# Kernel optimization log

Hardware: AMD Instinct MI355X
Metric: run time of the kernel (lower is better)

## Reference

```python
import jax, jax.numpy as jnp
import numpy as np

HEADS = 4
DIM_HEAD = 32
GROUPS = 32  # min(256//4, 32)
EPS = 1e-5


def setup_inputs() -> dict:
    key = jax.random.key(0)
    ks = jax.random.split(key, 6)
    B, C, H, W = 16, 256, 64, 64
    hidden = HEADS * DIM_HEAD  # 128
    return {
        "x": jax.random.normal(ks[0], (B, C, H, W), dtype=jnp.float32),
        "gn_w": jax.random.uniform(ks[1], (C,), dtype=jnp.float32),
        "gn_b": jax.random.normal(ks[2], (C,), dtype=jnp.float32) * 0.05,
        "qkv_w": jax.random.normal(ks[3], (3 * hidden, C), dtype=jnp.float32) * 0.05,
        "qkv_b": jax.random.normal(ks[4], (3 * hidden,), dtype=jnp.float32) * 0.05,
        "out_w": jax.random.normal(ks[5], (C, hidden), dtype=jnp.float32) * 0.05,
        "out_b": jnp.zeros((C,), dtype=jnp.float32),
    }


def _forward_single(x, gn_w, gn_b, qkv_w, qkv_b, out_w, out_b):
    # x: (c, h, w)
    c, h, w = x.shape
    # GroupNorm over (channels-in-group, h, w)
    xg = x.reshape(GROUPS, c // GROUPS, h, w)
    mean = xg.mean(axis=(1, 2, 3), keepdims=True)
    var = xg.var(axis=(1, 2, 3), keepdims=True)
    xn = ((xg - mean) * jax.lax.rsqrt(var + EPS)).reshape(c, h, w)
    xn = xn * gn_w[:, None, None] + gn_b[:, None, None]
    # 1x1 conv QKV projection
    qkv = jnp.einsum('oc,chw->ohw', qkv_w, xn) + qkv_b[:, None, None]
    qkv = qkv.reshape(3, HEADS, DIM_HEAD, h * w)
    q, k, v = qkv[0], qkv[1], qkv[2]
    k = jax.nn.softmax(k, axis=-1)  # softmax over spatial
    context = jnp.einsum('hdn,hen->hde', k, v)   # (heads, d, d)
    out = jnp.einsum('hde,hdn->hen', context, q)  # (heads, d, n)
    out = out.reshape(HEADS * DIM_HEAD, h, w)
    # 1x1 conv output projection
    return jnp.einsum('oc,chw->ohw', out_w, out) + out_b[:, None, None]


def reference(x, gn_w, gn_b, qkv_w, qkv_b, out_w, out_b):
    f = lambda xi: _forward_single(xi, gn_w, gn_b, qkv_w, qkv_b, out_w, out_b)
    return jax.vmap(f)(x)
```

## Files before the change

kernel.cpp:

```cpp
#include <hip/hip_runtime.h>
#include <stdint.h>

typedef unsigned short u16;
typedef __attribute__((ext_vector_type(8))) short bf16x8;
typedef __attribute__((ext_vector_type(4))) float f32x4;

#define B_   16
#define C_   256
#define HW_  4096
#define QR_  384
#define HID_ 128

__device__ __forceinline__ float b2f(u16 u) {
  union { uint32_t i; float f; } v; v.i = ((uint32_t)u) << 16; return v.f;
}
__device__ __forceinline__ u16 f2b(float f) {
  union { float f; uint32_t i; } v; v.f = f;
  uint32_t r = (v.i + 0x7FFFu + ((v.i >> 16) & 1u)) >> 16;
  return (u16)r;
}

__global__ __launch_bounds__(256) void gn_stats_conv_kernel(
    const float* __restrict__ x, const float* __restrict__ gnw,
    const float* __restrict__ gnb, float* __restrict__ scale,
    float* __restrict__ shiftv,
    const float* __restrict__ qkvw, u16* __restrict__ cqkvw)
{
  if (blockIdx.x >= 512) {
    int i = (blockIdx.x - 512) * 256 + threadIdx.x;
    float4 f = ((const float4*)qkvw)[i];
    ushort4 o;
    o.x = f2b(f.x); o.y = f2b(f.y); o.z = f2b(f.z); o.w = f2b(f.w);
    ((ushort4*)cqkvw)[i] = o;
    return;
  }
  int b = blockIdx.x >> 5, g = blockIdx.x & 31;
  const float* p = x + ((size_t)b * C_ + g * 8) * HW_;
  int t = threadIdx.x;
  float s = 0.f, sq = 0.f;
#pragma unroll
  for (int i = 0; i < 16; ++i) {
    float4 u0 = *(const float4*)(p + t * 8 + i * 2048);
    float4 u1 = *(const float4*)(p + t * 8 + i * 2048 + 4);
    s  += u0.x + u0.y + u0.z + u0.w + u1.x + u1.y + u1.z + u1.w;
    sq += u0.x*u0.x + u0.y*u0.y + u0.z*u0.z + u0.w*u0.w
        + u1.x*u1.x + u1.y*u1.y + u1.z*u1.z + u1.w*u1.w;
  }
#pragma unroll
  for (int off = 32; off > 0; off >>= 1) {
    s  += __shfl_down(s, off);
    sq += __shfl_down(sq, off);
  }
  __shared__ float ps[4], pq[4], mr[2];
  int lane = t & 63, w = t >> 6;
  if (lane == 0) { ps[w] = s; pq[w] = sq; }
  __syncthreads();
  if (t == 0) {
    float S = ps[0] + ps[1] + ps[2] + ps[3];
    float Q = pq[0] + pq[1] + pq[2] + pq[3];
    float mean = S * (1.f / 32768.f);
    float var  = Q * (1.f / 32768.f) - mean * mean;
    mr[0] = mean; mr[1] = rsqrtf(var + 1e-5f);
  }
  __syncthreads();
  if (t < 8) {
    int c = g * 8 + t;
    float sc = gnw[c] * mr[1];
    scale[b * C_ + c]  = sc;
    shiftv[b * C_ + c] = gnb[c] - mr[0] * sc;
  }
}

__global__ __launch_bounds__(256) void gn_transpose_kernel(
    const float* __restrict__ x, u16* __restrict__ dst,
    const float* __restrict__ scale, const float* __restrict__ shiftv)
{
  int nt = blockIdx.x, ct = blockIdx.y, b = blockIdx.z;
  const float* S = x + (size_t)b * C_ * HW_;
  u16* D = dst + (size_t)b * HW_ * C_;
  __shared__ __align__(16) u16 tile[64][136];
  int t = threadIdx.x;
  int n0 = nt * 128, c0 = ct * 64;
  int r = t >> 2, seg = (t & 3) * 32;
  float sc = scale[(size_t)b * C_ + c0 + r];
  float sh = shiftv[(size_t)b * C_ + c0 + r];
#pragma unroll
  for (int i = 0; i < 4; ++i) {
    const float* rp = S + (size_t)(c0 + r) * HW_ + n0 + seg + i * 8;
    float4 u0 = *(const float4*)(rp);
    float4 u1 = *(const float4*)(rp + 4);
    float f[8] = {u0.x, u0.y, u0.z, u0.w, u1.x, u1.y, u1.z, u1.w};
    uint4 o;
    uint32_t* op = (uint32_t*)&o;
#pragma unroll
    for (int j = 0; j < 4; ++j) {
      op[j] = (uint32_t)f2b(f[2 * j] * sc + sh)
            | ((uint32_t)f2b(f[2 * j + 1] * sc + sh) << 16);
    }
    *(uint4*)&tile[r][seg + i * 8] = o;
  }
  __syncthreads();
#pragma unroll
  for (int i = 0; i < 4; ++i) {
    int m = t * 4 + i;
    int n_l = m >> 3, cg = (m & 7) * 8;
    union { u16 v[8]; uint4 q; } pk;
#pragma unroll
    for (int e = 0; e < 8; ++e) pk.v[e] = tile[cg + e][n_l];
    *(uint4*)(D + (size_t)(n0 + n_l) * C_ + c0 + cg) = pk.q;
  }
}

__global__ __launch_bounds__(256) void q_gemm_kernel(
    const u16* __restrict__ A, const u16* __restrict__ Bt,
    const float* __restrict__ bias, u16* __restrict__ q_t)
{
  const int K = C_;
  int nt = blockIdx.x, b = blockIdx.y;
  const u16* Ab = A;
  const u16* Bb = Bt + (size_t)b * HW_ * C_ + (size_t)nt * 128 * K;
  __shared__ __align__(16) u16 smem[128 * 136];
  u16* lA = smem;
  u16* lB = smem + 8192;
  int t = threadIdx.x;
  int lane = t & 63, w = t >> 6;
  int quad = lane >> 4, l16 = lane & 15;
  int wm = (w >> 1) * 64, wn = (w & 1) * 64;
  f32x4 acc[4][4];
#pragma unroll
  for (int i = 0; i < 4; ++i)
#pragma unroll
    for (int j = 0; j < 4; ++j)
#pragma unroll
      for (int r = 0; r < 4; ++r) acc[i][j][r] = 0.f;

  for (int k0 = 0; k0 < K; k0 += 64) {
    __syncthreads();
#pragma unroll
    for (int q = 0; q < 4; ++q) {
      int ch = q * 256 + t;
      int row = ch >> 3, off = (ch & 7) * 8;
      __builtin_amdgcn_global_load_lds(
          (const __attribute__((address_space(1))) void*)(Ab + (size_t)row * K + k0 + off),
          (__attribute__((address_space(3))) void*)(lA + ch * 8), 16, 0, 0);
      __builtin_amdgcn_global_load_lds(
          (const __attribute__((address_space(1))) void*)(Bb + (size_t)row * K + k0 + off),
          (__attribute__((address_space(3))) void*)(lB + ch * 8), 16, 0, 0);
    }
    __syncthreads();
    const bf16x8* A8 = (const bf16x8*)lA;
    const bf16x8* B8 = (const bf16x8*)lB;
#pragma unroll
    for (int kk = 0; kk < 2; ++kk) {
      bf16x8 af[4], bfr[4];
#pragma unroll
      for (int i = 0; i < 4; ++i) af[i]  = A8[(wm + i * 16 + l16) * 8 + kk * 4 + quad];
#pragma unroll
      for (int j = 0; j < 4; ++j) bfr[j] = B8[(wn + j * 16 + l16) * 8 + kk * 4 + quad];
#pragma unroll
      for (int i = 0; i < 4; ++i)
#pragma unroll
        for (int j = 0; j < 4; ++j)
          acc[i][j] = __builtin_amdgcn_mfma_f32_16x16x32_bf16(af[i], bfr[j],
                                                              acc[i][j], 0, 0, 0);
    }
  }

  __syncthreads();
#pragma unroll
  for (int i = 0; i < 4; ++i) {
    int o0 = wm + i * 16 + quad * 4;
    float b0 = bias[o0], b1 = bias[o0 + 1], b2 = bias[o0 + 2], b3 = bias[o0 + 3];
#pragma unroll
    for (int j = 0; j < 4; ++j) {
      int n_l = wn + j * 16 + l16;
      uint2 pk;
      pk.x = (uint32_t)f2b(acc[i][j][0] + b0) | ((uint32_t)f2b(acc[i][j][1] + b1) << 16);
      pk.y = (uint32_t)f2b(acc[i][j][2] + b2) | ((uint32_t)f2b(acc[i][j][3] + b3) << 16);
      *(uint2*)&smem[n_l * 136 + o0] = pk;
    }
  }
  __syncthreads();
  int n_l = t >> 1, half = t & 1;
  u16* dst = q_t + (size_t)b * HW_ * HID_ + (size_t)(nt * 128 + n_l) * HID_ + half * 64;
  const u16* srcp = smem + n_l * 136 + half * 64;
#pragma unroll
  for (int i = 0; i < 8; ++i)
    *(uint4*)(dst + i * 8) = *(const uint4*)(srcp + i * 8);
}

__global__ __launch_bounds__(512) void kv_ctx_kernel(
    const u16* __restrict__ A,
    const u16* __restrict__ Bt,
    float* __restrict__ ctx_part,
    float* __restrict__ s_part)
{
  const int K = C_;
  int nt = blockIdx.x, b = blockIdx.y;
  const u16* Ab = A;
  const u16* Bb = Bt + (size_t)b * HW_ * C_ + (size_t)nt * 128 * K;
  __shared__ __align__(16) union {
    struct { u16 lA[256 * 64]; u16 lB[128 * 64]; } st;
    struct { u16 ek[128][136]; u16 vv[128][136]; float sred[2][128]; } ep;
    float cred[4096];
  } sm;
  int t = threadIdx.x;
  int lane = t & 63, w = t >> 6;
  int quad = lane >> 4, l16 = lane & 15;
  int wm = (w >> 1) * 64, wn = (w & 1) * 64;
  f32x4 acc[4][4];
#pragma unroll
  for (int i = 0; i < 4; ++i)
#pragma unroll
    for (int j = 0; j < 4; ++j)
#pragma unroll
      for (int r = 0; r < 4; ++r) acc[i][j][r] = 0.f;

  for (int k0 = 0; k0 < K; k0 += 64) {
    __syncthreads();
#pragma unroll
    for (int q = 0; q < 4; ++q) {
      int ch = q * 512 + t;
      int row = ch >> 3, off = (ch & 7) * 8;
      __builtin_amdgcn_global_load_lds(
          (const __attribute__((address_space(1))) void*)(Ab + (size_t)row * K + k0 + off),
          (__attribute__((address_space(3))) void*)(sm.st.lA + ch * 8), 16, 0, 0);
    }
#pragma unroll
    for (int q = 0; q < 2; ++q) {
      int ch = q * 512 + t;
      int row = ch >> 3, off = (ch & 7) * 8;
      __builtin_amdgcn_global_load_lds(
          (const __attribute__((address_space(1))) void*)(Bb + (size_t)row * K + k0 + off),
          (__attribute__((address_space(3))) void*)(sm.st.lB + ch * 8), 16, 0, 0);
    }
    __syncthreads();
    const bf16x8* A8 = (const bf16x8*)sm.st.lA;
    const bf16x8* B8 = (const bf16x8*)sm.st.lB;
#pragma unroll
    for (int kk = 0; kk < 2; ++kk) {
      bf16x8 af[4], bfr[4];
#pragma unroll
      for (int i = 0; i < 4; ++i) af[i]  = A8[(wm + i * 16 + l16) * 8 + kk * 4 + quad];
#pragma unroll
      for (int j = 0; j < 4; ++j) bfr[j] = B8[(wn + j * 16 + l16) * 8 + kk * 4 + quad];
#pragma unroll
      for (int i = 0; i < 4; ++i)
#pragma unroll
        for (int j = 0; j < 4; ++j)
          acc[i][j] = __builtin_amdgcn_mfma_f32_16x16x32_bf16(af[i], bfr[j],
                                                              acc[i][j], 0, 0, 0);
    }
  }

  __syncthreads();
  int h = w >> 1, nh = w & 1;
  if (w < 4) {
    float sl[4][4];
#pragma unroll
    for (int i = 0; i < 4; ++i)
#pragma unroll
      for (int r = 0; r < 4; ++r) sl[i][r] = 0.f;
#pragma unroll
    for (int i = 0; i < 4; ++i)
#pragma unroll
      for (int j = 0; j < 4; ++j)
#pragma unroll
        for (int r = 0; r < 4; ++r) {
          float e = __expf(acc[i][j][r]);
          sl[i][r] += e;
          sm.ep.ek[wm + i * 16 + quad * 4 + r][wn + j * 16 + l16] = f2b(e);
        }
#pragma unroll
    for (int i = 0; i < 4; ++i)
#pragma unroll
      for (int r = 0; r < 4; ++r) {
        float v = sl[i][r];
        v += __shfl_xor(v, 1);
        v += __shfl_xor(v, 2);
        v += __shfl_xor(v, 4);
        v += __shfl_xor(v, 8);
        if (l16 == 0) sm.ep.sred[nh][wm + i * 16 + quad * 4 + r] = v;
      }
  } else {
#pragma unroll
    for (int i = 0; i < 4; ++i)
#pragma unroll
      for (int j = 0; j < 4; ++j)
#pragma unroll
        for (int r = 0; r < 4; ++r)
          sm.ep.vv[wm - 128 + i * 16 + quad * 4 + r][wn + j * 16 + l16] =
              f2b(acc[i][j][r]);
  }
  __syncthreads();
  if (t < 128)
    s_part[((size_t)b * 32 + nt) * 128 + t] = sm.ep.sred[0][t] + sm.ep.sred[1][t];

  f32x4 c2[2][2];
#pragma unroll
  for (int i = 0; i < 2; ++i)
#pragma unroll
    for (int j = 0; j < 2; ++j)
#pragma unroll
      for (int r = 0; r < 4; ++r) c2[i][j][r] = 0.f;
#pragma unroll
  for (int kk = 0; kk < 2; ++kk) {
    bf16x8 ae[2], be[2];
#pragma unroll
    for (int i = 0; i < 2; ++i)
      ae[i] = *(const bf16x8*)&sm.ep.ek[h * 32 + i * 16 + l16][nh * 64 + kk * 32 + quad * 8];
#pragma unroll
    for (int j = 0; j < 2; ++j)
      be[j] = *(const bf16x8*)&sm.ep.vv[h * 32 + j * 16 + l16][nh * 64 + kk * 32 + quad * 8];
#pragma unroll
    for (int i = 0; i < 2; ++i)
#pragma unroll
      for (int j = 0; j < 2; ++j)
        c2[i][j] = __builtin_amdgcn_mfma_f32_16x16x32_bf16(ae[i], be[j], c2[i][j], 0, 0, 0);
  }
  __syncthreads();
  if (nh == 0) {
#pragma unroll
    for (int i = 0; i < 2; ++i)
#pragma unroll
      for (int j = 0; j < 2; ++j)
#pragma unroll
        for (int r = 0; r < 4; ++r)
          sm.cred[h * 1024 + (i * 16 + quad * 4 + r) * 32 + j * 16 + l16] = c2[i][j][r];
  }
  __syncthreads();
  if (nh == 1) {
#pragma unroll
    for (int i = 0; i < 2; ++i)
#pragma unroll
      for (int j = 0; j < 2; ++j)
#pragma unroll
        for (int r = 0; r < 4; ++r)
          sm.cred[h * 1024 + (i * 16 + quad * 4 + r) * 32 + j * 16 + l16] += c2[i][j][r];
  }
  __syncthreads();
  float4* dst = (float4*)(ctx_part + ((size_t)b * 32 + nt) * 4096);
  const float4* src4 = (const float4*)sm.cred;
  dst[t] = src4[t];
  dst[t + 512] = src4[t + 512];
}

__global__ __launch_bounds__(256) void fold_kernel(
    const float* __restrict__ ctx_part, const float* __restrict__ s_part,
    const float* __restrict__ outw, const float* __restrict__ qkvb,
    u16* __restrict__ wf)
{
  int b = blockIdx.x >> 2, h = blockIdx.x & 3;
  int t = threadIdx.x;
  __shared__ float cs[1024];
  __shared__ float sinv[32];
  const float* cp = ctx_part + ((size_t)b * 32) * 4096 + h * 1024;
  float4 aa = make_float4(0.f, 0.f, 0.f, 0.f);
  for (int ntb = 0; ntb < 32; ++ntb) {
    float4 v = *(const float4*)(cp + (size_t)ntb * 4096 + t * 4);
    aa.x += v.x; aa.y += v.y; aa.z += v.z; aa.w += v.w;
  }
  *(float4*)&cs[t * 4] = aa;
  if (t < 32) {
    float ssum = 0.f;
    for (int ntb = 0; ntb < 32; ++ntb)
      ssum += s_part[((size_t)b * 32 + ntb) * 128 + h * 32 + t];
    sinv[t] = 1.f / ssum;
  }
  __syncthreads();
  int o = t;
  const float* wr = outw + (size_t)o * HID_ + h * 32;
  float wv[32];
  float cb = 0.f;
#pragma unroll
  for (int e = 0; e < 32; ++e) {
    wv[e] = wr[e];
    cb += wv[e] * qkvb[256 + h * 32 + e];
  }
  union { u16 v[32]; uint4 q[4]; } pk;
#pragma unroll
  for (int d = 0; d < 32; ++d) {
    float a = 0.f;
#pragma unroll
    for (int e = 0; e < 32; ++e) a += wv[e] * cs[d * 32 + e];
    pk.v[d] = f2b(a * sinv[d] + cb);
  }
  uint4* dp = (uint4*)(wf + ((size_t)b * C_ + o) * HID_ + h * 32);
#pragma unroll
  for (int i = 0; i < 4; ++i) dp[i] = pk.q[i];
}

__global__ __launch_bounds__(256) void out_gemm_kernel(
    const u16* __restrict__ A, const u16* __restrict__ Bt,
    const float* __restrict__ bias, float* __restrict__ Cout)
{
  const int K = HID_;
  int nt = blockIdx.x, mt = blockIdx.y, b = blockIdx.z;
  const u16* Ab = A + (size_t)b * C_ * HID_ + (size_t)mt * 128 * K;
  const u16* Bb = Bt + (size_t)b * HW_ * HID_ + (size_t)nt * 128 * K;
  __shared__ __align__(16) u16 lA[128 * 64];
  __shared__ __align__(16) u16 lB[128 * 64];
  int t = threadIdx.x;
  int lane = t & 63, w = t >> 6;
  int quad = lane >> 4, l16 = lane & 15;
  int wm = (w >> 1) * 64, wn = (w & 1) * 64;
  f32x4 acc[4][4];
#pragma unroll
  for (int i = 0; i < 4; ++i)
#pragma unroll
    for (int j = 0; j < 4; ++j)
#pragma unroll
      for (int r = 0; r < 4; ++r) acc[i][j][r] = 0.f;

  for (int k0 = 0; k0 < K; k0 += 64) {
    __syncthreads();
#pragma unroll
    for (int q = 0; q < 4; ++q) {
      int ch = q * 256 + t;
      int row = ch >> 3, off = (ch & 7) * 8;
      __builtin_amdgcn_global_load_lds(
          (const __attribute__((address_space(1))) void*)(Ab + (size_t)row * K + k0 + off),
          (__attribute__((address_space(3))) void*)(lA + ch * 8), 16, 0, 0);
      __builtin_amdgcn_global_load_lds(
          (const __attribute__((address_space(1))) void*)(Bb + (size_t)row * K + k0 + off),
          (__attribute__((address_space(3))) void*)(lB + ch * 8), 16, 0, 0);
    }
    __syncthreads();
    const bf16x8* A8 = (const bf16x8*)lA;
    const bf16x8* B8 = (const bf16x8*)lB;
#pragma unroll
    for (int kk = 0; kk < 2; ++kk) {
      bf16x8 af[4], bfr[4];
#pragma unroll
      for (int i = 0; i < 4; ++i) af[i]  = A8[(wm + i * 16 + l16) * 8 + kk * 4 + quad];
#pragma unroll
      for (int j = 0; j < 4; ++j) bfr[j] = B8[(wn + j * 16 + l16) * 8 + kk * 4 + quad];
#pragma unroll
      for (int i = 0; i < 4; ++i)
#pragma unroll
        for (int j = 0; j < 4; ++j)
          acc[i][j] = __builtin_amdgcn_mfma_f32_16x16x32_bf16(af[i], bfr[j],
                                                              acc[i][j], 0, 0, 0);
    }
  }
#pragma unroll
  for (int i = 0; i < 4; ++i) {
#pragma unroll
    for (int rg = 0; rg < 4; ++rg) {
      int o = mt * 128 + wm + i * 16 + quad * 4 + rg;
      float bsv = bias[o];
      size_t rowbase = (size_t)b * C_ * HW_ + (size_t)o * HW_;
#pragma unroll
      for (int j = 0; j < 4; ++j) {
        int n = nt * 128 + wn + j * 16 + l16;
        Cout[rowbase + n] = acc[i][j][rg] + bsv;
      }
    }
  }
}

extern "C" void kernel_launch(void* const* d_in, const int* in_sizes, int n_in,
                              void* d_out, int out_size, void* d_ws, size_t ws_size,
                              hipStream_t stream)
{
  const float* x    = (const float*)d_in[0];
  const float* gnw  = (const float*)d_in[1];
  const float* gnb  = (const float*)d_in[2];
  const float* qkvw = (const float*)d_in[3];
  const float* qkvb = (const float*)d_in[4];
  const float* outw = (const float*)d_in[5];
  const float* outb = (const float*)d_in[6];

  char* p = (char*)d_ws;
  float* scale  = (float*)p;            p += (size_t)B_ * C_ * 4;
  float* shiftv = (float*)p;            p += (size_t)B_ * C_ * 4;
  u16* cqkvw = (u16*)p;                 p += (size_t)QR_ * C_ * 2;
  u16* xn_t  = (u16*)p;                 p += (size_t)B_ * HW_ * C_ * 2;
  u16* q_t   = (u16*)p;                 p += (size_t)B_ * HW_ * HID_ * 2;
  u16* wf    = (u16*)p;                 p += (size_t)B_ * C_ * HID_ * 2;
  float* ctxp = (float*)p;              p += (size_t)B_ * 32 * 4 * 1024 * 4;
  float* sp   = (float*)p;

  gn_stats_conv_kernel<<<608, 256, 0, stream>>>(x, gnw, gnb, scale, shiftv,
                                                qkvw, cqkvw);
  gn_transpose_kernel<<<dim3(32, 4, 16), 256, 0, stream>>>(x, xn_t, scale, shiftv);
  q_gemm_kernel<<<dim3(32, 16), 256, 0, stream>>>(cqkvw, xn_t, qkvb, q_t);
  kv_ctx_kernel<<<dim3(32, 16), 512, 0, stream>>>(cqkvw + 128 * C_, xn_t, ctxp, sp);
  fold_kernel<<<64, 256, 0, stream>>>(ctxp, sp, outw, qkvb, wf);
  out_gemm_kernel<<<dim3(32, 2, 16), 256, 0, stream>>>(wf, q_t, outb, (float*)d_out);
}
```

Before: 195.9 us.

## Fold Q projection into output GEMM and drop separate Q GEMM kernel

Removes the q_gemm kernel and its bf16 q_t intermediate. The output GEMM now computes the per-batch combined weight (Wf·Wq) on the fly for each K-slice via MFMA and multiplies it directly against the normalized input xn_t. The Q bias contribution is folded into a per-batch output bias produced in fold_kernel, and a transposed bf16 copy of Wq is prepared in the stats kernel. This trades one launch and a q_t round trip for redundant per-block weight-product MFMAs, a K of 256 instead of 128 in the output GEMM, and an extra rounding of the fused weights to bf16.

```diff
diff --git a/kernel.cpp b/kernel.cpp
--- a/kernel.cpp
+++ b/kernel.cpp
@@ -24,14 +24,35 @@
     const float* __restrict__ x, const float* __restrict__ gnw,
     const float* __restrict__ gnb, float* __restrict__ scale,
     float* __restrict__ shiftv,
-    const float* __restrict__ qkvw, u16* __restrict__ cqkvw)
+    const float* __restrict__ qkvw, u16* __restrict__ cqkvw,
+    u16* __restrict__ wqT)
 {
   if (blockIdx.x >= 512) {
-    int i = (blockIdx.x - 512) * 256 + threadIdx.x;
-    float4 f = ((const float4*)qkvw)[i];
-    ushort4 o;
-    o.x = f2b(f.x); o.y = f2b(f.y); o.z = f2b(f.z); o.w = f2b(f.w);
-    ((ushort4*)cqkvw)[i] = o;
+    int bi = blockIdx.x - 512;
+    int t = threadIdx.x;
+    if (bi < 96) {
+      int i = bi * 256 + t;
+      float4 f = ((const float4*)qkvw)[i];
+      ushort4 o;
+      o.x = f2b(f.x); o.y = f2b(f.y); o.z = f2b(f.z); o.w = f2b(f.w);
+      ((ushort4*)cqkvw)[i] = o;
+      return;
+    }
+    __shared__ u16 tl[16][272];
+    for (int j = 0; j < 8; ++j) {
+      int d = j * 16 + (t >> 4);
+      int cb = (t & 15) * 16;
+#pragma unroll
+      for (int ii = 0; ii < 16; ++ii)
+        tl[t >> 4][cb + ii] = f2b(qkvw[(size_t)d * 256 + cb + ii]);
+      __syncthreads();
+      union { u16 v[16]; uint4 q[2]; } pk;
+#pragma unroll
+      for (int dd = 0; dd < 16; ++dd) pk.v[dd] = tl[dd][t];
+      *(uint4*)(wqT + (size_t)t * 128 + j * 16)     = pk.q[0];
+      *(uint4*)(wqT + (size_t)t * 128 + j * 16 + 8) = pk.q[1];
+      __syncthreads();
+    }
     return;
   }
   int b = blockIdx.x >> 5, g = blockIdx.x & 31;
@@ -109,84 +130,6 @@
     for (int e = 0; e < 8; ++e) pk.v[e] = tile[cg + e][n_l];
     *(uint4*)(D + (size_t)(n0 + n_l) * C_ + c0 + cg) = pk.q;
   }
-}
-
-__global__ __launch_bounds__(256) void q_gemm_kernel(
-    const u16* __restrict__ A, const u16* __restrict__ Bt,
-    const float* __restrict__ bias, u16* __restrict__ q_t)
-{
-  const int K = C_;
-  int nt = blockIdx.x, b = blockIdx.y;
-  const u16* Ab = A;
-  const u16* Bb = Bt + (size_t)b * HW_ * C_ + (size_t)nt * 128 * K;
-  __shared__ __align__(16) u16 smem[128 * 136];
-  u16* lA = smem;
-  u16* lB = smem + 8192;
-  int t = threadIdx.x;
-  int lane = t & 63, w = t >> 6;
-  int quad = lane >> 4, l16 = lane & 15;
-  int wm = (w >> 1) * 64, wn = (w & 1) * 64;
-  f32x4 acc[4][4];
-#pragma unroll
-  for (int i = 0; i < 4; ++i)
-#pragma unroll
-    for (int j = 0; j < 4; ++j)
-#pragma unroll
-      for (int r = 0; r < 4; ++r) acc[i][j][r] = 0.f;
-
-  for (int k0 = 0; k0 < K; k0 += 64) {
-    __syncthreads();
-#pragma unroll
-    for (int q = 0; q < 4; ++q) {
-      int ch = q * 256 + t;
-      int row = ch >> 3, off = (ch & 7) * 8;
-      __builtin_amdgcn_global_load_lds(
-          (const __attribute__((address_space(1))) void*)(Ab + (size_t)row * K + k0 + off),
-          (__attribute__((address_space(3))) void*)(lA + ch * 8), 16, 0, 0);
-      __builtin_amdgcn_global_load_lds(
-          (const __attribute__((address_space(1))) void*)(Bb + (size_t)row * K + k0 + off),
-          (__attribute__((address_space(3))) void*)(lB + ch * 8), 16, 0, 0);
-    }
-    __syncthreads();
-    const bf16x8* A8 = (const bf16x8*)lA;
-    const bf16x8* B8 = (const bf16x8*)lB;
-#pragma unroll
-    for (int kk = 0; kk < 2; ++kk) {
-      bf16x8 af[4], bfr[4];
-#pragma unroll
-      for (int i = 0; i < 4; ++i) af[i]  = A8[(wm + i * 16 + l16) * 8 + kk * 4 + quad];
-#pragma unroll
-      for (int j = 0; j < 4; ++j) bfr[j] = B8[(wn + j * 16 + l16) * 8 + kk * 4 + quad];
-#pragma unroll
-      for (int i = 0; i < 4; ++i)
-#pragma unroll
-        for (int j = 0; j < 4; ++j)
-          acc[i][j] = __builtin_amdgcn_mfma_f32_16x16x32_bf16(af[i], bfr[j],
-                                                              acc[i][j], 0, 0, 0);
-    }
-  }
-
-  __syncthreads();
-#pragma unroll
-  for (int i = 0; i < 4; ++i) {
-    int o0 = wm + i * 16 + quad * 4;
-    float b0 = bias[o0], b1 = bias[o0 + 1], b2 = bias[o0 + 2], b3 = bias[o0 + 3];
-#pragma unroll
-    for (int j = 0; j < 4; ++j) {
-      int n_l = wn + j * 16 + l16;
-      uint2 pk;
-      pk.x = (uint32_t)f2b(acc[i][j][0] + b0) | ((uint32_t)f2b(acc[i][j][1] + b1) << 16);
-      pk.y = (uint32_t)f2b(acc[i][j][2] + b2) | ((uint32_t)f2b(acc[i][j][3] + b3) << 16);
-      *(uint2*)&smem[n_l * 136 + o0] = pk;
-    }
-  }
-  __syncthreads();
-  int n_l = t >> 1, half = t & 1;
-  u16* dst = q_t + (size_t)b * HW_ * HID_ + (size_t)(nt * 128 + n_l) * HID_ + half * 64;
-  const u16* srcp = smem + n_l * 136 + half * 64;
-#pragma unroll
-  for (int i = 0; i < 8; ++i)
-    *(uint4*)(dst + i * 8) = *(const uint4*)(srcp + i * 8);
 }
 
 __global__ __launch_bounds__(512) void kv_ctx_kernel(
@@ -348,7 +291,7 @@
 __global__ __launch_bounds__(256) void fold_kernel(
     const float* __restrict__ ctx_part, const float* __restrict__ s_part,
     const float* __restrict__ outw, const float* __restrict__ qkvb,
-    u16* __restrict__ wf)
+    u16* __restrict__ wf, float* __restrict__ btp)
 {
   int b = blockIdx.x >> 2, h = blockIdx.x & 3;
   int t = threadIdx.x;
@@ -378,32 +321,47 @@
     cb += wv[e] * qkvb[256 + h * 32 + e];
   }
   union { u16 v[32]; uint4 q[4]; } pk;
+  float bacc = 0.f;
 #pragma unroll
   for (int d = 0; d < 32; ++d) {
     float a = 0.f;
 #pragma unroll
     for (int e = 0; e < 32; ++e) a += wv[e] * cs[d * 32 + e];
-    pk.v[d] = f2b(a * sinv[d] + cb);
+    float val = a * sinv[d] + cb;
+    pk.v[d] = f2b(val);
+    bacc += val * qkvb[h * 32 + d];
   }
   uint4* dp = (uint4*)(wf + ((size_t)b * C_ + o) * HID_ + h * 32);
 #pragma unroll
   for (int i = 0; i < 4; ++i) dp[i] = pk.q[i];
+  btp[((size_t)b * 4 + h) * 256 + o] = bacc;
 }
 
 __global__ __launch_bounds__(256) void out_gemm_kernel(
-    const u16* __restrict__ A, const u16* __restrict__ Bt,
-    const float* __restrict__ bias, float* __restrict__ Cout)
-{
-  const int K = HID_;
+    const u16* __restrict__ wfp, const u16* __restrict__ wqT,
+    const u16* __restrict__ Bt, const float* __restrict__ outb,
+    const float* __restrict__ btp, float* __restrict__ Cout)
+{
   int nt = blockIdx.x, mt = blockIdx.y, b = blockIdx.z;
-  const u16* Ab = A + (size_t)b * C_ * HID_ + (size_t)mt * 128 * K;
-  const u16* Bb = Bt + (size_t)b * HW_ * HID_ + (size_t)nt * 128 * K;
+  const u16* wfB = wfp + (size_t)b * C_ * HID_ + (size_t)mt * 128 * HID_;
+  const u16* Bb  = Bt + (size_t)b * HW_ * C_ + (size_t)nt * 128 * C_;
+  __shared__ __align__(16) u16 lWF[128 * 128];
+  __shared__ __align__(16) u16 lWQ[64 * 128];
   __shared__ __align__(16) u16 lA[128 * 64];
   __shared__ __align__(16) u16 lB[128 * 64];
   int t = threadIdx.x;
   int lane = t & 63, w = t >> 6;
   int quad = lane >> 4, l16 = lane & 15;
   int wm = (w >> 1) * 64, wn = (w & 1) * 64;
+
+#pragma unroll
+  for (int q = 0; q < 8; ++q) {
+    int ch = q * 256 + t;
+    int row = ch >> 4, off = (ch & 15) * 8;
+    __builtin_amdgcn_global_load_lds(
+        (const __attribute__((address_space(1))) void*)(wfB + (size_t)row * HID_ + off),
+        (__attribute__((address_space(3))) void*)(lWF + ch * 8), 16, 0, 0);
+  }
   f32x4 acc[4][4];
 #pragma unroll
   for (int i = 0; i < 4; ++i)
@@ -412,18 +370,59 @@
 #pragma unroll
       for (int r = 0; r < 4; ++r) acc[i][j][r] = 0.f;
 
-  for (int k0 = 0; k0 < K; k0 += 64) {
+  for (int k0 = 0; k0 < C_; k0 += 64) {
     __syncthreads();
+#pragma unroll
+    for (int q = 0; q < 4; ++q) {
+      int ch = q * 256 + t;
+      int row = ch >> 4, off = (ch & 15) * 8;
+      __builtin_amdgcn_global_load_lds(
+          (const __attribute__((address_space(1))) void*)(wqT + (size_t)(k0 + row) * HID_ + off),
+          (__attribute__((address_space(3))) void*)(lWQ + ch * 8), 16, 0, 0);
+    }
 #pragma unroll
     for (int q = 0; q < 4; ++q) {
       int ch = q * 256 + t;
       int row = ch >> 3, off = (ch & 7) * 8;
       __builtin_amdgcn_global_load_lds(
-          (const __attribute__((address_space(1))) void*)(Ab + (size_t)row * K + k0 + off),
-          (__attribute__((address_space(3))) void*)(lA + ch * 8), 16, 0, 0);
-      __builtin_amdgcn_global_load_lds(
-          (const __attribute__((address_space(1))) void*)(Bb + (size_t)row * K + k0 + off),
+          (const __attribute__((address_space(1))) void*)(Bb + (size_t)row * C_ + k0 + off),
           (__attribute__((address_space(3))) void*)(lB + ch * 8), 16, 0, 0);
+    }
+    __syncthreads();
+    {
+      f32x4 facc[2][4];
+#pragma unroll
+      for (int i2 = 0; i2 < 2; ++i2)
+#pragma unroll
+        for (int j2 = 0; j2 < 4; ++j2)
+#pragma unroll
+          for (int r = 0; r < 4; ++r) facc[i2][j2][r] = 0.f;
+      const bf16x8* WF8 = (const bf16x8*)lWF;
+      const bf16x8* WQ8 = (const bf16x8*)lWQ;
+#pragma unroll
+      for (int kk = 0; kk < 4; ++kk) {
+        bf16x8 afv[2], bfv[4];
+#pragma unroll
+        for (int i2 = 0; i2 < 2; ++i2)
+          afv[i2] = WF8[(w * 32 + i2 * 16 + l16) * 16 + kk * 4 + quad];
+#pragma unroll
+        for (int j2 = 0; j2 < 4; ++j2)
+          bfv[j2] = WQ8[(j2 * 16 + l16) * 16 + kk * 4 + quad];
+#pragma unroll
+        for (int i2 = 0; i2 < 2; ++i2)
+#pragma unroll
+          for (int j2 = 0; j2 < 4; ++j2)
+            facc[i2][j2] = __builtin_amdgcn_mfma_f32_16x16x32_bf16(
+                afv[i2], bfv[j2], facc[i2][j2], 0, 0, 0);
+      }
+#pragma unroll
+      for (int i2 = 0; i2 < 2; ++i2)
+#pragma unroll
+        for (int j2 = 0; j2 < 4; ++j2)
+#pragma unroll
+          for (int r = 0; r < 4; ++r)
+            lA[(w * 32 + i2 * 16 + quad * 4 + r) * 64 + j2 * 16 + l16] =
+                f2b(facc[i2][j2][r]);
     }
     __syncthreads();
     const bf16x8* A8 = (const bf16x8*)lA;
@@ -448,7 +447,11 @@
 #pragma unroll
     for (int rg = 0; rg < 4; ++rg) {
       int o = mt * 128 + wm + i * 16 + quad * 4 + rg;
-      float bsv = bias[o];
+      float bsv = outb[o]
+                + btp[((size_t)b * 4 + 0) * 256 + o]
+                + btp[((size_t)b * 4 + 1) * 256 + o]
+                + btp[((size_t)b * 4 + 2) * 256 + o]
+                + btp[((size_t)b * 4 + 3) * 256 + o];
       size_t rowbase = (size_t)b * C_ * HW_ + (size_t)o * HW_;
 #pragma unroll
       for (int j = 0; j < 4; ++j) {
@@ -475,17 +478,18 @@
   float* scale  = (float*)p;            p += (size_t)B_ * C_ * 4;
   float* shiftv = (float*)p;            p += (size_t)B_ * C_ * 4;
   u16* cqkvw = (u16*)p;                 p += (size_t)QR_ * C_ * 2;
+  u16* wqT   = (u16*)p;                 p += (size_t)C_ * HID_ * 2;
   u16* xn_t  = (u16*)p;                 p += (size_t)B_ * HW_ * C_ * 2;
-  u16* q_t   = (u16*)p;                 p += (size_t)B_ * HW_ * HID_ * 2;
   u16* wf    = (u16*)p;                 p += (size_t)B_ * C_ * HID_ * 2;
   float* ctxp = (float*)p;              p += (size_t)B_ * 32 * 4 * 1024 * 4;
-  float* sp   = (float*)p;
-
-  gn_stats_conv_kernel<<<608, 256, 0, stream>>>(x, gnw, gnb, scale, shiftv,
-                                                qkvw, cqkvw);
+  float* sp   = (float*)p;              p += (size_t)B_ * 32 * 128 * 4;
+  float* btp  = (float*)p;
+
+  gn_stats_conv_kernel<<<609, 256, 0, stream>>>(x, gnw, gnb, scale, shiftv,
+                                                qkvw, cqkvw, wqT);
   gn_transpose_kernel<<<dim3(32, 4, 16), 256, 0, stream>>>(x, xn_t, scale, shiftv);
-  q_gemm_kernel<<<dim3(32, 16), 256, 0, stream>>>(cqkvw, xn_t, qkvb, q_t);
   kv_ctx_kernel<<<dim3(32, 16), 512, 0, stream>>>(cqkvw + 128 * C_, xn_t, ctxp, sp);
-  fold_kernel<<<64, 256, 0, stream>>>(ctxp, sp, outw, qkvb, wf);
-  out_gemm_kernel<<<dim3(32, 2, 16), 256, 0, stream>>>(wf, q_t, outb, (float*)d_out);
-}
+  fold_kernel<<<64, 256, 0, stream>>>(ctxp, sp, outw, qkvb, wf, btp);
+  out_gemm_kernel<<<dim3(32, 2, 16), 256, 0, stream>>>(wf, wqT, xn_t, outb, btp,
+                                                       (float*)d_out);
+}
```

After: 214.9 us. 1.1x slower.
